# Kernel optimization log

Hardware: AMD Instinct MI355X
Metric: run time of the kernel (lower is better)

## Reference

```python
import jax, jax.numpy as jnp
import numpy as np

B, T, S, H = 8, 256, 256, 512


def setup_inputs() -> dict:
    key = jax.random.key(0)
    k1, k2, k3, k4, k5, k6, k7 = jax.random.split(key, 7)
    query = jax.random.normal(k1, (B, T, H), dtype=jnp.float32)
    encoder_outputs = jax.random.normal(k2, (B, S, H), dtype=jnp.float32)
    src_lengths = jax.random.randint(k3, (B,), 1, S + 1)
    src_lengths = src_lengths.at[0].set(S)  # ensure max(lengths) == S (torch code masks to lengths.max())
    scale = 1.0 / np.sqrt(H)
    W_s = jax.random.normal(k4, (H, H), dtype=jnp.float32) * scale      # nn.Linear(H,H) weight
    W_h = jax.random.normal(k5, (H, H), dtype=jnp.float32) * scale
    v = jax.random.normal(k6, (H,), dtype=jnp.float32) * scale          # nn.Linear(H,1) weight
    W_out = jax.random.normal(k7, (H, 2 * H), dtype=jnp.float32) * scale  # nn.Linear(2H,H) weight
    return {"query": query, "encoder_outputs": encoder_outputs, "src_lengths": src_lengths,
            "W_s": W_s, "W_h": W_h, "v": v, "W_out": W_out}


def reference(query, encoder_outputs, src_lengths, W_s, W_h, v, W_out):
    # torch Linear: y = x @ W.T
    Ws_q = jnp.einsum('bth,oh->bto', query, W_s)            # (B,T,H)
    Wh_e = jnp.einsum('bsh,oh->bso', encoder_outputs, W_h)  # (B,S,H)
    # score(i,j) = v^T tanh(Ws_q_j + Wh_e_i), broadcast over (B,T,S,H)
    energies = jnp.einsum('btsh,h->bts',
                          jnp.tanh(Ws_q[:, :, None, :] + Wh_e[:, None, :, :]), v)
    mask = jnp.arange(encoder_outputs.shape[1]) < src_lengths[:, None]  # (B,S)
    energies = jnp.where(mask[:, None, :], energies, -jnp.inf)
    attn_weights = jax.nn.softmax(energies, axis=-1)        # (B,T,S)
    context = jnp.einsum('bts,bsh->bth', attn_weights, encoder_outputs)
    combined = jnp.concatenate([context, query], axis=-1)   # (B,T,2H)
    attn_out = jnp.tanh(jnp.einsum('btk,ok->bto', combined, W_out))
    return attn_out
```

## Files before the change

### kernel.cpp

```cpp
#include <hip/hip_runtime.h>
#include <hip/hip_bf16.h>


typedef __attribute__((ext_vector_type(8))) short bf16x8;
typedef __attribute__((ext_vector_type(4))) float floatx4;

#define C2LOG2E 2.8853900817779268f
#define LOG2E   1.4426950408889634f
#define NEGBIG  -1e30f

__device__ __forceinline__ float fexp2(float x) { return __builtin_amdgcn_exp2f(x); }
__device__ __forceinline__ float frcp(float x)  { return __builtin_amdgcn_rcpf(x); }
__device__ __forceinline__ float ftanh(float x) {
    return 1.0f - 2.0f * frcp(1.0f + fexp2(C2LOG2E * x));
}

__device__ __forceinline__ unsigned int f2bf_bits(float f) {
    unsigned int u = __float_as_uint(f);
    return (u + 0x7fffu + ((u >> 16) & 1u)) >> 16;
}

__global__ __launch_bounds__(256) void cast_all_bf16(
    const float* __restrict__ q,  const float* __restrict__ e,
    const float* __restrict__ Ws, const float* __restrict__ Wh,
    const float* __restrict__ Wo,
    unsigned short* __restrict__ qb,  unsigned short* __restrict__ eb,
    unsigned short* __restrict__ Wsb, unsigned short* __restrict__ Whb,
    unsigned short* __restrict__ Wob, float* __restrict__ E)
{
    int blk = blockIdx.x;
    if (blk >= 3072) {
        size_t i = ((size_t)(blk - 3072) * 256 + threadIdx.x) * 4;
        *(float4*)(E + i) = float4{0.f, 0.f, 0.f, 0.f};
        return;
    }
    const float* src; unsigned short* dst; int base;
    if      (blk < 1024) { src = q;  dst = qb;  base = blk; }
    else if (blk < 2048) { src = e;  dst = eb;  base = blk - 1024; }
    else if (blk < 2304) { src = Ws; dst = Wsb; base = blk - 2048; }
    else if (blk < 2560) { src = Wh; dst = Whb; base = blk - 2304; }
    else                 { src = Wo; dst = Wob; base = blk - 2560; }
    size_t i = (size_t)base * 1024 + threadIdx.x * 4;
    float4 f = *(const float4*)(src + i);
    ushort4 o;
    o.x = (unsigned short)f2bf_bits(f.x);
    o.y = (unsigned short)f2bf_bits(f.y);
    o.z = (unsigned short)f2bf_bits(f.z);
    o.w = (unsigned short)f2bf_bits(f.w);
    *(ushort4*)(dst + i) = o;
}

__global__ __launch_bounds__(256) void gemm64_tanh_dual(
    const unsigned short* __restrict__ X1, const unsigned short* __restrict__ W1,
    float* __restrict__ C1,
    const unsigned short* __restrict__ X2, const unsigned short* __restrict__ W2,
    float* __restrict__ C2)
{
    __shared__ unsigned short sA[64 * 72];
    __shared__ unsigned short sB[64 * 72];
    const int K = 512, N = 512;
    int blk = blockIdx.x;
    const unsigned short* X; const unsigned short* W; float* C;
    if (blk < 256) { X = X1; W = W1; C = C1; }
    else           { X = X2; W = W2; C = C2; blk -= 256; }
    int mt6 = blk >> 3, nt6 = blk & 7;
    int row0 = mt6 * 64, col0 = nt6 * 64;
    int tid = threadIdx.x, lane = tid & 63, w = tid >> 6;
    int srow = tid >> 2, sseg = (tid & 3) * 16;
    int mw = (w & 1) * 32, nw = (w >> 1) * 32;
    int r = lane & 15, kq = (lane >> 4) * 8;

    floatx4 acc00 = {0,0,0,0}, acc01 = {0,0,0,0}, acc10 = {0,0,0,0}, acc11 = {0,0,0,0};
    const unsigned short* ga = X + (size_t)(row0 + srow) * K + sseg;
    const unsigned short* gb = W + (size_t)(col0 + srow) * K + sseg;

    for (int kb = 0; kb < 8; ++kb) {
        uint4 a0 = *(const uint4*)(ga);
        uint4 a1 = *(const uint4*)(ga + 8);
        uint4 b0 = *(const uint4*)(gb);
        uint4 b1 = *(const uint4*)(gb + 8);
        ga += 64; gb += 64;
        __syncthreads();
        *(uint4*)&sA[srow * 72 + sseg]     = a0;
        *(uint4*)&sA[srow * 72 + sseg + 8] = a1;
        *(uint4*)&sB[srow * 72 + sseg]     = b0;
        *(uint4*)&sB[srow * 72 + sseg + 8] = b1;
        __syncthreads();
#pragma unroll
        for (int ks = 0; ks < 64; ks += 32) {
            bf16x8 af0 = *(const bf16x8*)&sA[(mw + r) * 72 + ks + kq];
            bf16x8 af1 = *(const bf16x8*)&sA[(mw + 16 + r) * 72 + ks + kq];
            bf16x8 bf0 = *(const bf16x8*)&sB[(nw + r) * 72 + ks + kq];
            bf16x8 bf1 = *(const bf16x8*)&sB[(nw + 16 + r) * 72 + ks + kq];
            acc00 = __builtin_amdgcn_mfma_f32_16x16x32_bf16(af0, bf0, acc00, 0, 0, 0);
            acc01 = __builtin_amdgcn_mfma_f32_16x16x32_bf16(af0, bf1, acc01, 0, 0, 0);
            acc10 = __builtin_amdgcn_mfma_f32_16x16x32_bf16(af1, bf0, acc10, 0, 0, 0);
            acc11 = __builtin_amdgcn_mfma_f32_16x16x32_bf16(af1, bf1, acc11, 0, 0, 0);
        }
    }
    int rq = (lane >> 4) * 4;
    float* cp = C + (size_t)(row0 + mw + rq) * N + col0 + nw + r;
#pragma unroll
    for (int i = 0; i < 4; ++i) {
        cp[(size_t)i * N]            = ftanh(acc00[i]);
        cp[(size_t)i * N + 16]       = ftanh(acc01[i]);
        cp[(size_t)(i + 16) * N]      = ftanh(acc10[i]);
        cp[(size_t)(i + 16) * N + 16] = ftanh(acc11[i]);
    }
}

#define HC 32
__global__ __launch_bounds__(512) void energies_partial(
    const float* __restrict__ Aq,
    const float* __restrict__ Bh,
    const float* __restrict__ Vv,
    const int* __restrict__ Len,
    float* __restrict__ E)
{
    __shared__ float sB[256][36];
    __shared__ float sA[8][36];
    __shared__ float sV[128];

    const int H = 512;
    int tid   = threadIdx.x;
    int lane  = tid & 63;
    int w     = tid >> 6;
    int b     = blockIdx.x >> 7;
    int hq    = (blockIdx.x >> 5) & 3;
    int ttile = blockIdx.x & 31;
    int row0g = b * 256 + ttile * 8;
    int len   = Len[b];
    int jmax  = (len + 63) >> 6;

    if (tid < 128) sV[tid] = Vv[hq * 128 + tid];

    float acc[4] = {0.f, 0.f, 0.f, 0.f};

    for (int hc = 0; hc < 128; hc += HC) {
        __syncthreads();
        {
            int row = tid >> 1;
            int cb  = (tid & 1) * 16;
            const float* src = Bh + (size_t)(b * 256 + row) * H + hq * 128 + hc + cb;
            float4 f0 = ((const float4*)src)[0];
            float4 f1 = ((const float4*)src)[1];
            float4 f2 = ((const float4*)src)[2];
            float4 f3 = ((const float4*)src)[3];
            float* dst = &sB[row][cb];
            *(float4*)(dst + 0)  = f0;
            *(float4*)(dst + 4)  = f1;
            *(float4*)(dst + 8)  = f2;
            *(float4*)(dst + 12) = f3;
        }
        if (tid < 256) {
            int row = tid >> 5, col = tid & 31;
            sA[row][col] = Aq[(size_t)(row0g + row) * H + hq * 128 + hc + col];
        }
        __syncthreads();

#pragma unroll
        for (int hh = 0; hh < HC; hh += 4) {
            float4 a4 = *(const float4*)&sA[w][hh];
            float4 v4 = *(const float4*)&sV[hc + hh];
#pragma unroll
            for (int j = 0; j < 4; ++j) {
                if (j < jmax) {
                    int s = lane + 64 * j;
                    float4 b4 = *(const float4*)&sB[s][hh];
                    acc[j] = fmaf(v4.x, (a4.x + b4.x) * frcp(fmaf(a4.x, b4.x, 1.0f)), acc[j]);
                    acc[j] = fmaf(v4.y, (a4.y + b4.y) * frcp(fmaf(a4.y, b4.y, 1.0f)), acc[j]);
                    acc[j] = fmaf(v4.z, (a4.z + b4.z) * frcp(fmaf(a4.z, b4.z, 1.0f)), acc[j]);
                    acc[j] = fmaf(v4.w, (a4.w + b4.w) * frcp(fmaf(a4.w, b4.w, 1.0f)), acc[j]);
                }
            }
        }
    }

    float* erow = E + (size_t)(row0g + w) * 256;
#pragma unroll
    for (int j = 0; j < 4; ++j)
        if (j < jmax) atomicAdd(erow + 64 * j + lane, acc[j]);
}

__global__ __launch_bounds__(512) void softmax_ctx_fused(
    const float* __restrict__ E,
    const unsigned short* __restrict__ Eb,
    const int* __restrict__ Len,
    unsigned short* __restrict__ Ctx)
{
    __shared__ unsigned short EncT[64][264];
    __shared__ unsigned short sWb[64][264];
    int tid = threadIdx.x, lane = tid & 63, w = tid >> 6;
    int blk = blockIdx.x;
    int b = blk & 7, hq = (blk >> 3) & 7, tg = blk >> 6;
    int len = Len[b];

    {
        int s = tid >> 1, hg = (tid & 1) * 32;
        const ushort4* src = (const ushort4*)(Eb + (size_t)(b * 256 + s) * 512 + hq * 64 + hg);
#pragma unroll
        for (int k = 0; k < 8; ++k) {
            ushort4 u = src[k];
            EncT[hg + k * 4 + 0][s] = u.x;
            EncT[hg + k * 4 + 1][s] = u.y;
            EncT[hg + k * 4 + 2][s] = u.z;
            EncT[hg + k * 4 + 3][s] = u.w;
        }
    }
    for (int i = 0; i < 8; ++i) {
        int row = w * 8 + i;
        const float* erow = E + (size_t)(b * 256 + tg * 64 + row) * 256;
        float ev[4];
#pragma unroll
        for (int j = 0; j < 4; ++j) {
            int s = lane + 64 * j;
            ev[j] = (s < len) ? erow[s] : NEGBIG;
        }
        float m = fmaxf(fmaxf(ev[0], ev[1]), fmaxf(ev[2], ev[3]));
#pragma unroll
        for (int o = 1; o < 64; o <<= 1) m = fmaxf(m, __shfl_xor(m, o, 64));
        float wv[4], wsum = 0.f;
#pragma unroll
        for (int j = 0; j < 4; ++j) { wv[j] = fexp2((ev[j] - m) * LOG2E); wsum += wv[j]; }
#pragma unroll
        for (int o = 1; o < 64; o <<= 1) wsum += __shfl_xor(wsum, o, 64);
        float inv = frcp(wsum);
#pragma unroll
        for (int j = 0; j < 4; ++j)
            sWb[row][lane + 64 * j] = (unsigned short)f2bf_bits(wv[j] * inv);
    }
    __syncthreads();

    int mt = w & 3, npair = w >> 2;
    int t0 = mt * 16;
    int r  = lane & 15, kq = (lane >> 4) * 8;
    int n0 = npair * 32 + r;
    floatx4 acc0 = {0.f,0.f,0.f,0.f}, acc1 = {0.f,0.f,0.f,0.f};
#pragma unroll
    for (int k = 0; k < 8; ++k) {
        bf16x8 a  = *(const bf16x8*)(&sWb[t0 + r][kq + 32 * k]);
        bf16x8 b0 = *(const bf16x8*)(&EncT[n0][kq + 32 * k]);
        bf16x8 b1 = *(const bf16x8*)(&EncT[n0 + 16][kq + 32 * k]);
        acc0 = __builtin_amdgcn_mfma_f32_16x16x32_bf16(a, b0, acc0, 0, 0, 0);
        acc1 = __builtin_amdgcn_mfma_f32_16x16x32_bf16(a, b1, acc1, 0, 0, 0);
    }
    int row0 = (lane >> 4) * 4;
    unsigned short* op = Ctx + (size_t)(b * 256 + tg * 64 + t0 + row0) * 512 + hq * 64 + npair * 32 + r;
#pragma unroll
    for (int i = 0; i < 4; ++i) {
        op[i * 512]      = (unsigned short)f2bf_bits(acc0[i]);
        op[i * 512 + 16] = (unsigned short)f2bf_bits(acc1[i]);
    }
}

__global__ __launch_bounds__(256) void out_gemm64_tanh(
    const unsigned short* __restrict__ Ctx, const unsigned short* __restrict__ Q,
    const unsigned short* __restrict__ Wout, float* __restrict__ Out)
{
    __shared__ unsigned short sA[64 * 72];
    __shared__ unsigned short sB[64 * 72];
    const int N = 512, KW = 1024;
    int blk = blockIdx.x;
    int mt6 = blk >> 3, nt6 = blk & 7;
    int row0 = mt6 * 64, col0 = nt6 * 64;
    int tid = threadIdx.x, lane = tid & 63, w = tid >> 6;
    int srow = tid >> 2, sseg = (tid & 3) * 16;
    int mw = (w & 1) * 32, nw = (w >> 1) * 32;
    int r = lane & 15, kq = (lane >> 4) * 8;

    floatx4 acc00 = {0,0,0,0}, acc01 = {0,0,0,0}, acc10 = {0,0,0,0}, acc11 = {0,0,0,0};
    const unsigned short* gb = Wout + (size_t)(col0 + srow) * KW + sseg;

    for (int kb = 0; kb < 16; ++kb) {
        const unsigned short* asrc = (kb < 8 ? Ctx : Q);
        const unsigned short* ga = asrc + (size_t)(row0 + srow) * 512 + (kb & 7) * 64 + sseg;
        uint4 a0 = *(const uint4*)(ga);
        uint4 a1 = *(const uint4*)(ga + 8);
        uint4 b0 = *(const uint4*)(gb);
        uint4 b1 = *(const uint4*)(gb + 8);
        gb += 64;
        __syncthreads();
        *(uint4*)&sA[srow * 72 + sseg]     = a0;
        *(uint4*)&sA[srow * 72 + sseg + 8] = a1;
        *(uint4*)&sB[srow * 72 + sseg]     = b0;
        *(uint4*)&sB[srow * 72 + sseg + 8] = b1;
        __syncthreads();
#pragma unroll
        for (int ks = 0; ks < 64; ks += 32) {
            bf16x8 af0 = *(const bf16x8*)&sA[(mw + r) * 72 + ks + kq];
            bf16x8 af1 = *(const bf16x8*)&sA[(mw + 16 + r) * 72 + ks + kq];
            bf16x8 bf0 = *(const bf16x8*)&sB[(nw + r) * 72 + ks + kq];
            bf16x8 bf1 = *(const bf16x8*)&sB[(nw + 16 + r) * 72 + ks + kq];
            acc00 = __builtin_amdgcn_mfma_f32_16x16x32_bf16(af0, bf0, acc00, 0, 0, 0);
            acc01 = __builtin_amdgcn_mfma_f32_16x16x32_bf16(af0, bf1, acc01, 0, 0, 0);
            acc10 = __builtin_amdgcn_mfma_f32_16x16x32_bf16(af1, bf0, acc10, 0, 0, 0);
            acc11 = __builtin_amdgcn_mfma_f32_16x16x32_bf16(af1, bf1, acc11, 0, 0, 0);
        }
    }
    int rq = (lane >> 4) * 4;
    float* op = Out + (size_t)(row0 + mw + rq) * N + col0 + nw + r;
#pragma unroll
    for (int i = 0; i < 4; ++i) {
        op[(size_t)i * N]             = ftanh(acc00[i]);
        op[(size_t)i * N + 16]        = ftanh(acc01[i]);
        op[(size_t)(i + 16) * N]      = ftanh(acc10[i]);
        op[(size_t)(i + 16) * N + 16] = ftanh(acc11[i]);
    }
}

extern "C" void kernel_launch(void* const* d_in, const int* in_sizes, int n_in,
                              void* d_out, int out_size, void* d_ws, size_t ws_size,
                              hipStream_t stream)
{
    const float* query = (const float*)d_in[0];
    const float* enc   = (const float*)d_in[1];
    const int*   len   = (const int*)d_in[2];
    const float* Ws    = (const float*)d_in[3];
    const float* Wh    = (const float*)d_in[4];
    const float* v     = (const float*)d_in[5];
    const float* Wout  = (const float*)d_in[6];
    float* out = (float*)d_out;

    float* wsq = (float*)d_ws;
    float* whe = wsq + 2048 * 512;
    float* E   = whe + 2048 * 512;
    unsigned short* ctx = (unsigned short*)wsq;
    unsigned short* qb  = (unsigned short*)(E + 2048 * 256);
    unsigned short* eb  = qb + 2048 * 512;
    unsigned short* Wsb = eb + 2048 * 512;
    unsigned short* Whb = Wsb + 512 * 512;
    unsigned short* Wob = Whb + 512 * 512;

    cast_all_bf16<<<3584, 256, 0, stream>>>(query, enc, Ws, Wh, Wout,
                                            qb, eb, Wsb, Whb, Wob, E);
    gemm64_tanh_dual<<<512, 256, 0, stream>>>(qb, Wsb, wsq, eb, Whb, whe);
    energies_partial<<<1024, 512, 0, stream>>>(wsq, whe, v, len, E);
    softmax_ctx_fused<<<256, 512, 0, stream>>>(E, eb, len, ctx);
    out_gemm64_tanh<<<256, 256, 0, stream>>>(ctx, qb, Wob, out);
}
```

Before: 138.8 us.

## Replace energy atomics with per-slice partial buffers, pair rcp ops, skip masked rows

Energies kernel now writes each H-quarter's partial sums to its own buffer instead of atomically adding into a zeroed E, and the softmax kernel sums the four partials. This removes the zero-fill blocks and the atomics. The tanh-of-sum identity is evaluated two terms at a time so one reciprocal serves two products, halving rcp work in the hot loop. Shared loads of encoder rows now skip rows beyond the batch length. It costs extra workspace and four reads per energy element, and the paired products may overflow or lose precision.

Result: no change. 137.4 us (-1.0%).

```diff
diff --git a/kernel.cpp b/kernel.cpp
--- a/kernel.cpp
+++ b/kernel.cpp
@@ -26,14 +26,9 @@
     const float* __restrict__ Wo,
     unsigned short* __restrict__ qb,  unsigned short* __restrict__ eb,
     unsigned short* __restrict__ Wsb, unsigned short* __restrict__ Whb,
-    unsigned short* __restrict__ Wob, float* __restrict__ E)
+    unsigned short* __restrict__ Wob)
 {
     int blk = blockIdx.x;
-    if (blk >= 3072) {
-        size_t i = ((size_t)(blk - 3072) * 256 + threadIdx.x) * 4;
-        *(float4*)(E + i) = float4{0.f, 0.f, 0.f, 0.f};
-        return;
-    }
     const float* src; unsigned short* dst; int base;
     if      (blk < 1024) { src = q;  dst = qb;  base = blk; }
     else if (blk < 2048) { src = e;  dst = eb;  base = blk - 1024; }
@@ -102,8 +97,8 @@
     float* cp = C + (size_t)(row0 + mw + rq) * N + col0 + nw + r;
 #pragma unroll
     for (int i = 0; i < 4; ++i) {
-        cp[(size_t)i * N]            = ftanh(acc00[i]);
-        cp[(size_t)i * N + 16]       = ftanh(acc01[i]);
+        cp[(size_t)i * N]             = ftanh(acc00[i]);
+        cp[(size_t)i * N + 16]        = ftanh(acc01[i]);
         cp[(size_t)(i + 16) * N]      = ftanh(acc10[i]);
         cp[(size_t)(i + 16) * N + 16] = ftanh(acc11[i]);
     }
@@ -115,7 +110,7 @@
     const float* __restrict__ Bh,
     const float* __restrict__ Vv,
     const int* __restrict__ Len,
-    float* __restrict__ E)
+    float* __restrict__ E4)
 {
     __shared__ float sB[256][36];
     __shared__ float sA[8][36];
@@ -139,18 +134,13 @@
     for (int hc = 0; hc < 128; hc += HC) {
         __syncthreads();
         {
-            int row = tid >> 1;
-            int cb  = (tid & 1) * 16;
-            const float* src = Bh + (size_t)(b * 256 + row) * H + hq * 128 + hc + cb;
-            float4 f0 = ((const float4*)src)[0];
-            float4 f1 = ((const float4*)src)[1];
-            float4 f2 = ((const float4*)src)[2];
-            float4 f3 = ((const float4*)src)[3];
-            float* dst = &sB[row][cb];
-            *(float4*)(dst + 0)  = f0;
-            *(float4*)(dst + 4)  = f1;
-            *(float4*)(dst + 8)  = f2;
-            *(float4*)(dst + 12) = f3;
+            int rr = tid >> 3;
+            int cc = (tid & 7) * 4;
+            for (int jj = 0; jj < jmax; ++jj) {
+                int row = jj * 64 + rr;
+                float4 f = *(const float4*)(Bh + (size_t)(b * 256 + row) * H + hq * 128 + hc + cc);
+                *(float4*)&sB[row][cc] = f;
+            }
         }
         if (tid < 256) {
             int row = tid >> 5, col = tid & 31;
@@ -167,23 +157,29 @@
                 if (j < jmax) {
                     int s = lane + 64 * j;
                     float4 b4 = *(const float4*)&sB[s][hh];
-                    acc[j] = fmaf(v4.x, (a4.x + b4.x) * frcp(fmaf(a4.x, b4.x, 1.0f)), acc[j]);
-                    acc[j] = fmaf(v4.y, (a4.y + b4.y) * frcp(fmaf(a4.y, b4.y, 1.0f)), acc[j]);
-                    acc[j] = fmaf(v4.z, (a4.z + b4.z) * frcp(fmaf(a4.z, b4.z, 1.0f)), acc[j]);
-                    acc[j] = fmaf(v4.w, (a4.w + b4.w) * frcp(fmaf(a4.w, b4.w, 1.0f)), acc[j]);
+                    float n0 = a4.x + b4.x, n1 = a4.y + b4.y;
+                    float n2 = a4.z + b4.z, n3 = a4.w + b4.w;
+                    float d0 = fmaf(a4.x, b4.x, 1.0f), d1 = fmaf(a4.y, b4.y, 1.0f);
+                    float d2 = fmaf(a4.z, b4.z, 1.0f), d3 = fmaf(a4.w, b4.w, 1.0f);
+                    float x0 = v4.x * n0, x1 = v4.y * n1;
+                    float x2 = v4.z * n2, x3 = v4.w * n3;
+                    float num01 = fmaf(x1, d0, x0 * d1);
+                    float num23 = fmaf(x3, d2, x2 * d3);
+                    acc[j] = fmaf(num01, frcp(d0 * d1), acc[j]);
+                    acc[j] = fmaf(num23, frcp(d2 * d3), acc[j]);
                 }
             }
         }
     }
 
-    float* erow = E + (size_t)(row0g + w) * 256;
+    float* erow = E4 + ((size_t)hq * 2048 + row0g + w) * 256;
 #pragma unroll
     for (int j = 0; j < 4; ++j)
-        if (j < jmax) atomicAdd(erow + 64 * j + lane, acc[j]);
+        if (j < jmax) erow[64 * j + lane] = acc[j];
 }
 
 __global__ __launch_bounds__(512) void softmax_ctx_fused(
-    const float* __restrict__ E,
+    const float* __restrict__ E4,
     const unsigned short* __restrict__ Eb,
     const int* __restrict__ Len,
     unsigned short* __restrict__ Ctx)
@@ -209,12 +205,15 @@
     }
     for (int i = 0; i < 8; ++i) {
         int row = w * 8 + i;
-        const float* erow = E + (size_t)(b * 256 + tg * 64 + row) * 256;
+        size_t grow = (size_t)(b * 256 + tg * 64 + row) * 256;
         float ev[4];
 #pragma unroll
         for (int j = 0; j < 4; ++j) {
             int s = lane + 64 * j;
-            ev[j] = (s < len) ? erow[s] : NEGBIG;
+            float sum = E4[grow + s] + E4[(size_t)2048 * 256 + grow + s]
+                      + E4[(size_t)2 * 2048 * 256 + grow + s]
+                      + E4[(size_t)3 * 2048 * 256 + grow + s];
+            ev[j] = (s < len) ? sum : NEGBIG;
         }
         float m = fmaxf(fmaxf(ev[0], ev[1]), fmaxf(ev[2], ev[3]));
 #pragma unroll
@@ -323,18 +322,18 @@
 
     float* wsq = (float*)d_ws;
     float* whe = wsq + 2048 * 512;
-    float* E   = whe + 2048 * 512;
-    unsigned short* ctx = (unsigned short*)wsq;
-    unsigned short* qb  = (unsigned short*)(E + 2048 * 256);
+    float* E4  = whe + 2048 * 512;
+    unsigned short* qb  = (unsigned short*)(E4 + 4 * 2048 * 256);
     unsigned short* eb  = qb + 2048 * 512;
     unsigned short* Wsb = eb + 2048 * 512;
     unsigned short* Whb = Wsb + 512 * 512;
     unsigned short* Wob = Whb + 512 * 512;
-
-    cast_all_bf16<<<3584, 256, 0, stream>>>(query, enc, Ws, Wh, Wout,
-                                            qb, eb, Wsb, Whb, Wob, E);
+    unsigned short* ctx = Wob + 512 * 1024;
+
+    cast_all_bf16<<<3072, 256, 0, stream>>>(query, enc, Ws, Wh, Wout,
+                                            qb, eb, Wsb, Whb, Wob);
     gemm64_tanh_dual<<<512, 256, 0, stream>>>(qb, Wsb, wsq, eb, Whb, whe);
-    energies_partial<<<1024, 512, 0, stream>>>(wsq, whe, v, len, E);
-    softmax_ctx_fused<<<256, 512, 0, stream>>>(E, eb, len, ctx);
+    energies_partial<<<1024, 512, 0, stream>>>(wsq, whe, v, len, E4);
+    softmax_ctx_fused<<<256, 512, 0, stream>>>(E4, eb, len, ctx);
     out_gemm64_tanh<<<256, 256, 0, stream>>>(ctx, qb, Wob, out);
 }
```
